# Performance work log

Measured on AMD Instinct MI355X. Metric: run time of the kernel, lower is better.

The kernel has to match this reference:

```python
import jax, jax.numpy as jnp
import numpy as np

TS = 0.1
ECNUM = 1024
CA1NUM = 1024
CA3NUM = 1024
CA3SIGMA = 5.0
TRACKLEN = 100
ACTNUM = 2
BS = 8192
CUELOC = int(0.1 * TRACKLEN)  # sensory cue injected at this step
NOISE_P = 0.04 * TS           # per-step EC3 spontaneous-spike probability


def _xavier_std(fan_in, fan_out):
    return float(np.sqrt(2.0 / (fan_in + fan_out)))


def setup_inputs() -> dict:
    key = jax.random.key(0)
    ks = jax.random.split(key, 6)
    cue = jax.random.normal(ks[0], (BS, ECNUM), jnp.float32)
    ec5_init = jax.random.uniform(ks[1], (BS, ECNUM), jnp.float32)
    wca3ca1 = jax.random.uniform(ks[2], (CA3NUM, CA1NUM), jnp.float32) * 0.01
    wec3ca1 = jax.random.normal(ks[3], (ECNUM, CA1NUM), jnp.float32) * _xavier_std(ECNUM, CA1NUM)
    wca1ec5 = jax.random.normal(ks[4], (CA1NUM, ECNUM), jnp.float32) * _xavier_std(CA1NUM, ECNUM)
    wca1act = jax.random.normal(ks[5], (CA1NUM, ACTNUM), jnp.float32) * _xavier_std(CA1NUM, ACTNUM)
    ca1bias = jnp.zeros((CA1NUM,), jnp.float32)
    ec5bias = jnp.zeros((ECNUM,), jnp.float32)
    actbias = jnp.zeros((ACTNUM,), jnp.float32)
    return {"cue": cue, "ec5_init": ec5_init, "wca3ca1": wca3ca1,
            "wec3ca1": wec3ca1, "wca1ec5": wca1ec5, "wca1act": wca1act,
            "ca1bias": ca1bias, "ec5bias": ec5bias, "actbias": actbias}


def _forward(cue, ec5_init, wca3ca1, wec3ca1, wca1ec5, wca1act, ca1bias, ec5bias, actbias):
    bs = cue.shape[0]
    dt = cue.dtype
    # CA3 place-cell tuning curves for all positions: (T, ca3num)
    ca3center = jnp.linspace(0.0, TRACKLEN, CA3NUM).astype(dt)
    xs = jnp.arange(TRACKLEN)
    ca3_all = jnp.exp(-((ca3center[None, :] - xs[:, None].astype(dt)) ** 2)
                      / (2.0 * CA3SIGMA ** 2))
    drive = ca3_all @ wca3ca1            # (T, ca1num), precomputed CA3->CA1 drive
    cue_mask = (xs == CUELOC).astype(dt)  # (T,)
    noise_key = jax.random.key(42)

    ec3_0 = jnp.zeros((bs, ECNUM), dt)
    ca1_0 = jnp.zeros((bs, CA1NUM), dt)

    def step(carry, inp):
        ec3, ec5, _ = carry
        d, m, t = inp
        ca1 = jax.nn.relu(d[None, :] * (1.0 + jax.nn.sigmoid(ec3 @ wec3ca1)) - ca1bias)
        ec5 = ec5 + (10.0 * TS) * (ca1 @ wca1ec5) + ec5bias
        ec5 = 0.5 + 0.5 * jax.nn.sigmoid(4.0 * (ec5 - 0.5))
        ec3 = ec5 * ec3 + m * cue
        k = jax.random.fold_in(noise_key, t)
        ec3 = ec3 + 0.2 * jax.random.bernoulli(k, NOISE_P, (bs, ECNUM)).astype(dt)
        return (ec3, ec5, ca1), None

    (ec3, ec5, ca1), _ = jax.lax.scan(step, (ec3_0, ec5_init, ca1_0),
                                      (drive, cue_mask, xs))
    return ca1 @ wca1act + actbias       # (bs, actnum)


def reference(cue, ec5_init, wca3ca1, wec3ca1, wca1ec5, wca1act, ca1bias, ec5bias, actbias):
    return _forward(cue, ec5_init, wca3ca1, wec3ca1, wca1ec5, wca1act,
                    ca1bias, ec5bias, actbias)
```

## Files before the change

kernel.cpp:

```cpp
#include <hip/hip_runtime.h>
#include <stdint.h>

#define BS 8192
#define NDIM 1024
#define T_STEPS 100
#define CUE_T 10
#define BK 64
#define NKT (NDIM / BK)

typedef __attribute__((ext_vector_type(8))) short bf16x8;
typedef __attribute__((ext_vector_type(16))) float f32x16;

__device__ inline uint16_t f32_to_bf16(float f) {
    uint32_t u = __float_as_uint(f);
    uint32_t r = u + 0x7fffu + ((u >> 16) & 1u);
    return (uint16_t)(r >> 16);
}
__device__ inline float bf16_to_f32(uint16_t h) {
    return __uint_as_float(((uint32_t)h) << 16);
}

__host__ __device__ inline uint32_t rotl32_(uint32_t x, uint32_t r) {
    return (x << r) | (x >> (32u - r));
}

__host__ __device__ inline void tf2x32(uint32_t k0, uint32_t k1,
                                       uint32_t x0, uint32_t x1,
                                       uint32_t &o0, uint32_t &o1) {
    uint32_t ks2 = k0 ^ k1 ^ 0x1BD11BDAu;
    x0 += k0; x1 += k1;
#define TF_R4(a,b,c,d) \
    x0 += x1; x1 = rotl32_(x1,(a)); x1 ^= x0; \
    x0 += x1; x1 = rotl32_(x1,(b)); x1 ^= x0; \
    x0 += x1; x1 = rotl32_(x1,(c)); x1 ^= x0; \
    x0 += x1; x1 = rotl32_(x1,(d)); x1 ^= x0;
    TF_R4(13,15,26,6)  x0 += k1;  x1 += ks2 + 1u;
    TF_R4(17,29,16,24) x0 += ks2; x1 += k0 + 2u;
    TF_R4(13,15,26,6)  x0 += k0;  x1 += k1 + 3u;
    TF_R4(17,29,16,24) x0 += k1;  x1 += ks2 + 4u;
    TF_R4(13,15,26,6)  x0 += ks2; x1 += k0 + 5u;
#undef TF_R4
    o0 = x0; o1 = x1;
}

__device__ __forceinline__ void tf2x32_x4_fold(uint32_t k0, uint32_t k1,
                                               const uint32_t idx[4],
                                               uint32_t bits[4]) {
    uint32_t ks2 = k0 ^ k1 ^ 0x1BD11BDAu;
    uint32_t x0[4], x1[4];
    #pragma unroll
    for (int i = 0; i < 4; ++i) { x0[i] = k0; x1[i] = idx[i] + k1; }
#define TF4_R(rot) \
    _Pragma("unroll") \
    for (int i = 0; i < 4; ++i) { \
        x0[i] += x1[i]; x1[i] = rotl32_(x1[i], (rot)); x1[i] ^= x0[i]; }
#define TF4_K(a0, a1) \
    _Pragma("unroll") \
    for (int i = 0; i < 4; ++i) { x0[i] += (a0); x1[i] += (a1); }
    TF4_R(13) TF4_R(15) TF4_R(26) TF4_R(6)  TF4_K(k1, ks2 + 1u)
    TF4_R(17) TF4_R(29) TF4_R(16) TF4_R(24) TF4_K(ks2, k0 + 2u)
    TF4_R(13) TF4_R(15) TF4_R(26) TF4_R(6)  TF4_K(k0, k1 + 3u)
    TF4_R(17) TF4_R(29) TF4_R(16) TF4_R(24) TF4_K(k1, ks2 + 4u)
    TF4_R(13) TF4_R(15) TF4_R(26) TF4_R(6)  TF4_K(ks2, k0 + 5u)
#undef TF4_R
#undef TF4_K
    #pragma unroll
    for (int i = 0; i < 4; ++i) bits[i] = x0[i] ^ x1[i];
}

__device__ inline float sigmoidf_(float x) {
    float e = __expf(-x);
    return __builtin_amdgcn_rcpf(1.0f + e);
}

__device__ __forceinline__ void gload16(const uint16_t* g, uint16_t* l) {
    __builtin_amdgcn_global_load_lds(
        (const __attribute__((address_space(1))) void*)g,
        (__attribute__((address_space(3))) void*)l, 16, 0, 0);
}

__global__ void init_kernel(const float* __restrict__ ec5_init,
                            uint16_t* __restrict__ ec3bf,
                            uint16_t* __restrict__ ec5bf, int n) {
    int i = blockIdx.x * blockDim.x + threadIdx.x;
    if (i < n) { ec3bf[i] = 0; ec5bf[i] = f32_to_bf16(ec5_init[i]); }
}

__global__ __launch_bounds__(256) void drive_kernel(const float* __restrict__ W,
                                                    float* __restrict__ drive) {
    __shared__ float g[4][1024];
    const int t0 = blockIdx.x * 4;
    const int c = blockIdx.y * 64 + (threadIdx.x & 63);
    const int tt = threadIdx.x >> 6;
    const float stepf = 100.0f / 1023.0f;
    for (int i = threadIdx.x; i < 4096; i += 256) {
        int t_ = i >> 10, j = i & 1023;
        float d = stepf * (float)j - (float)(t0 + t_);
        g[t_][j] = expf(-(d * d) * 0.02f);
    }
    __syncthreads();
    float a = 0.f;
    for (int j = 0; j < 1024; ++j)
        a = fmaf(g[tt][j], W[(size_t)j * NDIM + c], a);
    drive[(size_t)(t0 + tt) * NDIM + c] = a;
}

__global__ __launch_bounds__(256) void wtrans_kernel(const float* __restrict__ W,
                                                     uint16_t* __restrict__ Wt) {
    __shared__ float tile[32][33];
    int k0 = blockIdx.x * 32, n0 = blockIdx.y * 32;
    int tx = threadIdx.x & 31, ty = threadIdx.x >> 5;
    #pragma unroll
    for (int i = 0; i < 32; i += 8)
        tile[ty + i][tx] = W[(size_t)(k0 + ty + i) * NDIM + n0 + tx];
    __syncthreads();
    #pragma unroll
    for (int i = 0; i < 32; i += 8)
        Wt[(size_t)(n0 + ty + i) * NDIM + k0 + tx] = f32_to_bf16(tile[tx][ty + i]);
}

template<bool NOISE>
__device__ __forceinline__ void gemm_core_t(const uint16_t* __restrict__ A,
                                            const uint16_t* __restrict__ Bt,
                                            uint16_t* As, uint16_t* Bs,
                                            f32x16 acc[2],
                                            uint32_t k0_, uint32_t k1_,
                                            uint32_t obase, uint32_t &mask) {
    const int tid = threadIdx.x;
    const int wid = tid >> 6, lane = tid & 63;
    const int row0 = blockIdx.x * 128, col0 = blockIdx.y * 128;
    const int ch0 = tid, ch1 = tid + 512;
    const int r0c = ch0 >> 3, r1c = ch1 >> 3;
    const int s0 = ((ch0 & 7) ^ (r0c & 7)) << 3;
    const int s1 = ((ch1 & 7) ^ (r1c & 7)) << 3;
    const uint16_t* aS0 = A  + (size_t)(row0 + r0c) * NDIM + s0;
    const uint16_t* aS1 = A  + (size_t)(row0 + r1c) * NDIM + s1;
    const uint16_t* bS0 = Bt + (size_t)(col0 + r0c) * NDIM + s0;
    const uint16_t* bS1 = Bt + (size_t)(col0 + r1c) * NDIM + s1;
    const int l31 = lane & 31, l5 = lane >> 5;
    const int wr = wid >> 1, wc = wid & 1;
    const int ar = wr * 32 + l31;
    int aoff[4], boff[2][4];
    #pragma unroll
    for (int kk = 0; kk < 4; ++kk) {
        aoff[kk] = ar * BK + ((((kk << 1) | l5) ^ (ar & 7)) << 3);
        #pragma unroll
        for (int n = 0; n < 2; ++n) {
            int br = wc * 64 + n * 32 + l31;
            boff[n][kk] = br * BK + ((((kk << 1) | l5) ^ (br & 7)) << 3);
        }
    }

    gload16(aS0, As + ch0 * 8);
    gload16(aS1, As + ch1 * 8);
    gload16(bS0, Bs + ch0 * 8);
    gload16(bS1, Bs + ch1 * 8);

    for (int kt = 0; kt < NKT; ++kt) {
        const int cur = kt & 1;
        if (kt + 1 < NKT) {
            const int nb = (cur ^ 1) * 8192;
            const int k0n = (kt + 1) * BK;
            gload16(aS0 + k0n, As + nb + ch0 * 8);
            gload16(aS1 + k0n, As + nb + ch1 * 8);
            gload16(bS0 + k0n, Bs + nb + ch0 * 8);
            gload16(bS1 + k0n, Bs + nb + ch1 * 8);
            asm volatile("s_waitcnt vmcnt(4)" ::: "memory");
        } else {
            asm volatile("s_waitcnt vmcnt(0)" ::: "memory");
        }
        __builtin_amdgcn_s_barrier();
        __builtin_amdgcn_sched_barrier(0);
        const uint16_t* as = As + cur * 8192;
        const uint16_t* bs = Bs + cur * 8192;
        bf16x8 af[4], bfr[2][4];
        #pragma unroll
        for (int kk = 0; kk < 4; ++kk) {
            af[kk] = *(const bf16x8*)&as[aoff[kk]];
            #pragma unroll
            for (int n = 0; n < 2; ++n)
                bfr[n][kk] = *(const bf16x8*)&bs[boff[n][kk]];
        }
        #pragma unroll
        for (int kk = 0; kk < 4; ++kk)
            #pragma unroll
            for (int n = 0; n < 2; ++n)
                acc[n] = __builtin_amdgcn_mfma_f32_32x32x16_bf16(
                    af[kk], bfr[n][kk], acc[n], 0, 0, 0);
        if (NOISE && !(kt & 1)) {
            uint32_t idx[4], bits[4];
            #pragma unroll
            for (int u = 0; u < 4; ++u) {
                int e = (kt << 1) + u;
                idx[u] = obase + (uint32_t)((e >> 3) << 15) + (uint32_t)(e & 7);
            }
            tf2x32_x4_fold(k0_, k1_, idx, bits);
            #pragma unroll
            for (int u = 0; u < 4; ++u) {
                float uu = __uint_as_float((bits[u] >> 9) | 0x3f800000u) - 1.0f;
                mask |= (uint32_t)(uu < 0.004f ? 1u : 0u) << ((kt << 1) + u);
            }
        }
        __builtin_amdgcn_sched_barrier(0);
        __builtin_amdgcn_s_barrier();
    }
}

__device__ __forceinline__ void acc_to_lds(float* lacc, f32x16 acc[2]) {
    const int tid = threadIdx.x, wid = tid >> 6, lane = tid & 63;
    const int wr = wid >> 1, wc = wid & 1, l31 = lane & 31, l5 = lane >> 5;
    #pragma unroll
    for (int n = 0; n < 2; ++n) {
        int c = wc * 64 + n * 32 + l31;
        int chunk = c >> 2, cj = c & 3;
        #pragma unroll
        for (int e = 0; e < 16; ++e) {
            int r = wr * 32 + (e & 3) + ((e >> 2) << 3) + (l5 << 2);
            lacc[r * 128 + ((chunk ^ (r & 31)) << 2) + cj] = acc[n][e];
        }
    }
}

__device__ __forceinline__ void acc_read8(const float* lacc, int r, int a,
                                          float4 &v0, float4 &v1) {
    int rb = r & 31;
    v0 = *(const float4*)&lacc[r * 128 + ((((a << 1) | 0) ^ rb) << 2)];
    v1 = *(const float4*)&lacc[r * 128 + ((((a << 1) | 1) ^ rb) << 2)];
}

__global__ __launch_bounds__(512, 4) void gemm1_kernel(
    const uint16_t* __restrict__ ec3bf, const uint16_t* __restrict__ W1t,
    const float* __restrict__ drv, const float* __restrict__ bias,
    uint16_t* __restrict__ ca1bf, float* __restrict__ ca1f, int writef32,
    uint32_t* __restrict__ maskbuf, uint32_t k0_, uint32_t k1_)
{
    __shared__ __align__(16) uint16_t SM[2][16384];
    uint16_t* As = SM[0];
    uint16_t* Bs = SM[1];
    f32x16 acc[2];
    acc[0] = (f32x16)(0.0f);
    acc[1] = (f32x16)(0.0f);

    const int tid = threadIdx.x;
    const int row0 = blockIdx.x * 128, col0 = blockIdx.y * 128;
    const int a = tid & 15;
    const uint32_t obase = (uint32_t)(row0 + (tid >> 4)) * NDIM
                         + (uint32_t)(col0 + a * 8);
    uint32_t mask = 0;
    gemm_core_t<true>(ec3bf, W1t, As, Bs, acc, k0_, k1_, obase, mask);

    maskbuf[(size_t)(blockIdx.y * 64 + blockIdx.x) * 512 + tid] = mask;

    float* lacc = (float*)SM;
    acc_to_lds(lacc, acc);
    __syncthreads();

    int gc = col0 + a * 8;
    float4 d0 = *(const float4*)&drv[gc];
    float4 d1 = *(const float4*)&drv[gc + 4];
    float4 b0 = *(const float4*)&bias[gc];
    float4 b1 = *(const float4*)&bias[gc + 4];
    #pragma unroll
    for (int i = 0; i < 4; ++i) {
        int r = (tid >> 4) + i * 32;
        float4 v0, v1;
        acc_read8(lacc, r, a, v0, v1);
        size_t off = (size_t)(row0 + r) * NDIM + gc;
        float vout[8];
        #pragma unroll
        for (int j = 0; j < 8; ++j) {
            float accv = j < 4 ? v0[j] : v1[j - 4];
            float dv = j < 4 ? d0[j] : d1[j - 4];
            float bi = j < 4 ? b0[j] : b1[j - 4];
            float s = sigmoidf_(accv);
            float v = dv * (1.0f + s) - bi;
            vout[j] = v > 0.0f ? v : 0.0f;
        }
        bf16x8 pk;
        #pragma unroll
        for (int j = 0; j < 8; ++j) pk[j] = (short)f32_to_bf16(vout[j]);
        *(bf16x8*)&ca1bf[off] = pk;
        if (writef32) {
            float4 f0 = {vout[0], vout[1], vout[2], vout[3]};
            float4 f1 = {vout[4], vout[5], vout[6], vout[7]};
            *(float4*)&ca1f[off] = f0;
            *(float4*)&ca1f[off + 4] = f1;
        }
    }
}

__global__ __launch_bounds__(512, 4) void gemm2_kernel(
    const uint16_t* __restrict__ ca1bf, const uint16_t* __restrict__ W2t,
    const float* __restrict__ cue, const float* __restrict__ bias,
    uint16_t* __restrict__ ec3bf, uint16_t* __restrict__ ec5bf,
    const uint32_t* __restrict__ maskbuf, int inject)
{
    __shared__ __align__(16) uint16_t SM[2][16384];
    uint16_t* As = SM[0];
    uint16_t* Bs = SM[1];
    f32x16 acc[2];
    acc[0] = (f32x16)(0.0f);
    acc[1] = (f32x16)(0.0f);

    const int tid = threadIdx.x;
    const int row0 = blockIdx.x * 128, col0 = blockIdx.y * 128;
    const int a = tid & 15;
    const uint32_t mask = maskbuf[(size_t)(blockIdx.y * 64 + blockIdx.x) * 512 + tid];

    uint32_t dummy = 0;
    gemm_core_t<false>(ca1bf, W2t, As, Bs, acc, 0u, 0u, 0u, dummy);

    bf16x8 e3v[4], e5v[4];
    #pragma unroll
    for (int i = 0; i < 4; ++i) {
        size_t off = (size_t)(row0 + (tid >> 4) + i * 32) * NDIM + col0 + a * 8;
        e3v[i] = *(const bf16x8*)&ec3bf[off];
        e5v[i] = *(const bf16x8*)&ec5bf[off];
    }

    float* lacc = (float*)SM;
    acc_to_lds(lacc, acc);
    __syncthreads();

    int gc = col0 + a * 8;
    float4 b0 = *(const float4*)&bias[gc];
    float4 b1 = *(const float4*)&bias[gc + 4];
    #pragma unroll
    for (int i = 0; i < 4; ++i) {
        int r = (tid >> 4) + i * 32;
        float4 v0, v1;
        acc_read8(lacc, r, a, v0, v1);
        size_t off = (size_t)(row0 + r) * NDIM + gc;
        float4 c0 = {0.f,0.f,0.f,0.f}, c1 = {0.f,0.f,0.f,0.f};
        if (inject) {
            c0 = *(const float4*)&cue[off];
            c1 = *(const float4*)&cue[off + 4];
        }
        bf16x8 p3, p5;
        #pragma unroll
        for (int j = 0; j < 8; ++j) {
            float accv = j < 4 ? v0[j] : v1[j - 4];
            float bi = j < 4 ? b0[j] : b1[j - 4];
            float e5 = bf16_to_f32((uint16_t)e5v[i][j]);
            float e3 = bf16_to_f32((uint16_t)e3v[i][j]);
            float u = e5 + accv + bi;
            float e5n = 0.5f + 0.5f * sigmoidf_(4.0f * (u - 0.5f));
            float e3n = e5n * e3;
            if (inject) e3n += (j < 4 ? c0[j] : c1[j - 4]);
            e3n += ((mask >> (i * 8 + j)) & 1u) ? 0.2f : 0.0f;
            p5[j] = (short)f32_to_bf16(e5n);
            p3[j] = (short)f32_to_bf16(e3n);
        }
        *(bf16x8*)&ec5bf[off] = p5;
        *(bf16x8*)&ec3bf[off] = p3;
    }
}

__global__ __launch_bounds__(256) void final_kernel(
    const float* __restrict__ ca1,
    const float* __restrict__ wact,
    const float* __restrict__ actbias,
    float* __restrict__ out)
{
    int wave = threadIdx.x >> 6, lane = threadIdx.x & 63;
    int b = blockIdx.x * 4 + wave;
    double a0 = 0.0, a1 = 0.0;
    for (int c = lane; c < NDIM; c += 64) {
        double v = (double)ca1[(size_t)b * NDIM + c];
        a0 += v * (double)wact[c * 2 + 0];
        a1 += v * (double)wact[c * 2 + 1];
    }
    #pragma unroll
    for (int off = 32; off > 0; off >>= 1) {
        a0 += __shfl_down(a0, off);
        a1 += __shfl_down(a1, off);
    }
    if (lane == 0) {
        out[(size_t)b * 2 + 0] = (float)(a0 + (double)actbias[0]);
        out[(size_t)b * 2 + 1] = (float)(a1 + (double)actbias[1]);
    }
}

extern "C" void kernel_launch(void* const* d_in, const int* in_sizes, int n_in,
                              void* d_out, int out_size, void* d_ws, size_t ws_size,
                              hipStream_t stream) {
    const float* cue      = (const float*)d_in[0];
    const float* ec5_init = (const float*)d_in[1];
    const float* wca3ca1  = (const float*)d_in[2];
    const float* wec3ca1  = (const float*)d_in[3];
    const float* wca1ec5  = (const float*)d_in[4];
    const float* wca1act  = (const float*)d_in[5];
    const float* ca1bias  = (const float*)d_in[6];
    const float* ec5bias  = (const float*)d_in[7];
    const float* actbias  = (const float*)d_in[8];
    float* out = (float*)d_out;

    const size_t NE = (size_t)BS * NDIM;
    char* p = (char*)d_ws;
    float*    ca1f    = (float*)p;    p += NE * 4;
    uint16_t* ec3bf   = (uint16_t*)p; p += NE * 2;
    uint16_t* ec5bf   = (uint16_t*)p; p += NE * 2;
    uint16_t* ca1bf   = (uint16_t*)p; p += NE * 2;
    uint16_t* W1t     = (uint16_t*)p; p += (size_t)NDIM * NDIM * 2;
    uint16_t* W2t     = (uint16_t*)p; p += (size_t)NDIM * NDIM * 2;
    uint32_t* maskbuf = (uint32_t*)p; p += (size_t)512 * 512 * 4;
    float*    drive   = (float*)p;

    const int n = (int)NE;
    hipLaunchKernelGGL(init_kernel, dim3((n + 255) / 256), dim3(256), 0, stream,
                       ec5_init, ec3bf, ec5bf, n);
    hipLaunchKernelGGL(drive_kernel, dim3(25, 16), dim3(256), 0, stream,
                       wca3ca1, drive);
    hipLaunchKernelGGL(wtrans_kernel, dim3(32, 32), dim3(256), 0, stream, wec3ca1, W1t);
    hipLaunchKernelGGL(wtrans_kernel, dim3(32, 32), dim3(256), 0, stream, wca1ec5, W2t);

    dim3 blk(512);
    dim3 gg(BS / 128, NDIM / 128);
    for (int t = 0; t < T_STEPS; ++t) {
        uint32_t k0, k1;
        tf2x32(0u, 42u, 0u, (uint32_t)t, k0, k1);
        hipLaunchKernelGGL(gemm1_kernel, gg, blk, 0, stream,
                           ec3bf, W1t, drive + (size_t)t * NDIM, ca1bias,
                           ca1bf, ca1f, (t == T_STEPS - 1) ? 1 : 0,
                           maskbuf, k0, k1);
        if (t < T_STEPS - 1) {
            hipLaunchKernelGGL(gemm2_kernel, gg, blk, 0, stream,
                               ca1bf, W2t, cue, ec5bias, ec3bf, ec5bf,
                               maskbuf, (t == CUE_T) ? 1 : 0);
        }
    }
    hipLaunchKernelGGL(final_kernel, dim3(BS / 4), dim3(256), 0, stream,
                       ca1f, wca1act, actbias, out);
}
```

Baseline: 6.559 ms.

## Shrink GEMM tiles to 128x64 with BK=32 and 256-thread blocks

Retiles both step GEMMs from 128x128 tiles with 512 threads and BK=64 to 128x64 tiles with 256 threads and BK=32. Each wave now computes a 64x32 sub-tile, and LDS shrinks to 32KB per block, so more blocks can be resident and the grid holds twice as many blocks. The noise-mask generation, LDS swizzles, epilogue indexing and mask buffer layout are remapped to match. In exchange there is less data reuse per tile, more K iterations with more barriers, and more global traffic for the A operand.

```diff
diff --git a/kernel.cpp b/kernel.cpp
--- a/kernel.cpp
+++ b/kernel.cpp
@@ -5,7 +5,7 @@
 #define NDIM 1024
 #define T_STEPS 100
 #define CUE_T 10
-#define BK 64
+#define BK 32
 #define NKT (NDIM / BK)
 
 typedef __attribute__((ext_vector_type(8))) short bf16x8;
@@ -122,83 +122,81 @@
 template<bool NOISE>
 __device__ __forceinline__ void gemm_core_t(const uint16_t* __restrict__ A,
                                             const uint16_t* __restrict__ Bt,
-                                            uint16_t* As, uint16_t* Bs,
+                                            uint16_t* SM,
                                             f32x16 acc[2],
                                             uint32_t k0_, uint32_t k1_,
                                             uint32_t obase, uint32_t &mask) {
     const int tid = threadIdx.x;
     const int wid = tid >> 6, lane = tid & 63;
-    const int row0 = blockIdx.x * 128, col0 = blockIdx.y * 128;
-    const int ch0 = tid, ch1 = tid + 512;
-    const int r0c = ch0 >> 3, r1c = ch1 >> 3;
-    const int s0 = ((ch0 & 7) ^ (r0c & 7)) << 3;
-    const int s1 = ((ch1 & 7) ^ (r1c & 7)) << 3;
-    const uint16_t* aS0 = A  + (size_t)(row0 + r0c) * NDIM + s0;
-    const uint16_t* aS1 = A  + (size_t)(row0 + r1c) * NDIM + s1;
-    const uint16_t* bS0 = Bt + (size_t)(col0 + r0c) * NDIM + s0;
-    const uint16_t* bS1 = Bt + (size_t)(col0 + r1c) * NDIM + s1;
+    const int row0 = blockIdx.x * 128, col0 = blockIdx.y * 64;
+    uint16_t* As = SM;
+    uint16_t* Bs = SM + 8192;
+
+    const int soff = (((tid & 3) ^ ((tid >> 2) & 3))) << 3;
+    const uint16_t* aS0 = A  + (size_t)(row0 + (tid >> 2)) * NDIM + soff;
+    const uint16_t* aS1 = A  + (size_t)(row0 + (tid >> 2) + 64) * NDIM + soff;
+    const uint16_t* bS0 = Bt + (size_t)(col0 + (tid >> 2)) * NDIM + soff;
+
     const int l31 = lane & 31, l5 = lane >> 5;
     const int wr = wid >> 1, wc = wid & 1;
-    const int ar = wr * 32 + l31;
-    int aoff[4], boff[2][4];
-    #pragma unroll
-    for (int kk = 0; kk < 4; ++kk) {
-        aoff[kk] = ar * BK + ((((kk << 1) | l5) ^ (ar & 7)) << 3);
-        #pragma unroll
-        for (int n = 0; n < 2; ++n) {
-            int br = wc * 64 + n * 32 + l31;
-            boff[n][kk] = br * BK + ((((kk << 1) | l5) ^ (br & 7)) << 3);
-        }
-    }
-
-    gload16(aS0, As + ch0 * 8);
-    gload16(aS1, As + ch1 * 8);
-    gload16(bS0, Bs + ch0 * 8);
-    gload16(bS1, Bs + ch1 * 8);
+    int aoff[2][2], boff[2];
+    #pragma unroll
+    for (int kk = 0; kk < 2; ++kk) {
+        #pragma unroll
+        for (int m = 0; m < 2; ++m) {
+            int ar = wr * 64 + m * 32 + l31;
+            aoff[m][kk] = ar * BK + ((((kk << 1) | l5) ^ (ar & 3)) << 3);
+        }
+        int br = wc * 32 + l31;
+        boff[kk] = br * BK + ((((kk << 1) | l5) ^ (br & 3)) << 3);
+    }
+
+    gload16(aS0, As + tid * 8);
+    gload16(aS1, As + (tid + 256) * 8);
+    gload16(bS0, Bs + tid * 8);
 
     for (int kt = 0; kt < NKT; ++kt) {
         const int cur = kt & 1;
         if (kt + 1 < NKT) {
-            const int nb = (cur ^ 1) * 8192;
             const int k0n = (kt + 1) * BK;
-            gload16(aS0 + k0n, As + nb + ch0 * 8);
-            gload16(aS1 + k0n, As + nb + ch1 * 8);
-            gload16(bS0 + k0n, Bs + nb + ch0 * 8);
-            gload16(bS1 + k0n, Bs + nb + ch1 * 8);
-            asm volatile("s_waitcnt vmcnt(4)" ::: "memory");
+            uint16_t* An = As + (cur ^ 1) * 4096;
+            uint16_t* Bn = Bs + (cur ^ 1) * 2048;
+            gload16(aS0 + k0n, An + tid * 8);
+            gload16(aS1 + k0n, An + (tid + 256) * 8);
+            gload16(bS0 + k0n, Bn + tid * 8);
+            asm volatile("s_waitcnt vmcnt(3)" ::: "memory");
         } else {
             asm volatile("s_waitcnt vmcnt(0)" ::: "memory");
         }
         __builtin_amdgcn_s_barrier();
         __builtin_amdgcn_sched_barrier(0);
-        const uint16_t* as = As + cur * 8192;
-        const uint16_t* bs = Bs + cur * 8192;
-        bf16x8 af[4], bfr[2][4];
-        #pragma unroll
-        for (int kk = 0; kk < 4; ++kk) {
-            af[kk] = *(const bf16x8*)&as[aoff[kk]];
+        const uint16_t* as = As + cur * 4096;
+        const uint16_t* bs = Bs + cur * 2048;
+        bf16x8 af[2][2], bfr[2];
+        #pragma unroll
+        for (int kk = 0; kk < 2; ++kk) {
+            af[0][kk] = *(const bf16x8*)&as[aoff[0][kk]];
+            af[1][kk] = *(const bf16x8*)&as[aoff[1][kk]];
+            bfr[kk]   = *(const bf16x8*)&bs[boff[kk]];
+        }
+        #pragma unroll
+        for (int kk = 0; kk < 2; ++kk)
             #pragma unroll
-            for (int n = 0; n < 2; ++n)
-                bfr[n][kk] = *(const bf16x8*)&bs[boff[n][kk]];
-        }
-        #pragma unroll
-        for (int kk = 0; kk < 4; ++kk)
+            for (int m = 0; m < 2; ++m)
+                acc[m] = __builtin_amdgcn_mfma_f32_32x32x16_bf16(
+                    af[m][kk], bfr[kk], acc[m], 0, 0, 0);
+        if (NOISE && !(kt & 3)) {
+            const int b = kt >> 2;
+            uint32_t idx[4], bits[4];
+            const uint32_t base = obase + (uint32_t)((b >> 1) << 15)
+                                + (uint32_t)((b & 1) << 2);
             #pragma unroll
-            for (int n = 0; n < 2; ++n)
-                acc[n] = __builtin_amdgcn_mfma_f32_32x32x16_bf16(
-                    af[kk], bfr[n][kk], acc[n], 0, 0, 0);
-        if (NOISE && !(kt & 1)) {
-            uint32_t idx[4], bits[4];
-            #pragma unroll
-            for (int u = 0; u < 4; ++u) {
-                int e = (kt << 1) + u;
-                idx[u] = obase + (uint32_t)((e >> 3) << 15) + (uint32_t)(e & 7);
-            }
+            for (int u = 0; u < 4; ++u) idx[u] = base + u;
             tf2x32_x4_fold(k0_, k1_, idx, bits);
             #pragma unroll
             for (int u = 0; u < 4; ++u) {
                 float uu = __uint_as_float((bits[u] >> 9) | 0x3f800000u) - 1.0f;
-                mask |= (uint32_t)(uu < 0.004f ? 1u : 0u) << ((kt << 1) + u);
+                mask |= (uint32_t)(uu < 0.004f ? 1u : 0u) << ((b << 2) + u);
             }
         }
         __builtin_amdgcn_sched_barrier(0);
@@ -209,47 +207,44 @@
 __device__ __forceinline__ void acc_to_lds(float* lacc, f32x16 acc[2]) {
     const int tid = threadIdx.x, wid = tid >> 6, lane = tid & 63;
     const int wr = wid >> 1, wc = wid & 1, l31 = lane & 31, l5 = lane >> 5;
-    #pragma unroll
-    for (int n = 0; n < 2; ++n) {
-        int c = wc * 64 + n * 32 + l31;
-        int chunk = c >> 2, cj = c & 3;
+    const int c = wc * 32 + l31;
+    const int chunk = c >> 2, cj = c & 3;
+    #pragma unroll
+    for (int m = 0; m < 2; ++m)
         #pragma unroll
         for (int e = 0; e < 16; ++e) {
-            int r = wr * 32 + (e & 3) + ((e >> 2) << 3) + (l5 << 2);
-            lacc[r * 128 + ((chunk ^ (r & 31)) << 2) + cj] = acc[n][e];
-        }
-    }
+            int r = wr * 64 + m * 32 + (e & 3) + ((e >> 2) << 3) + (l5 << 2);
+            lacc[r * 64 + ((chunk ^ (r & 15)) << 2) + cj] = acc[m][e];
+        }
 }
 
 __device__ __forceinline__ void acc_read8(const float* lacc, int r, int a,
                                           float4 &v0, float4 &v1) {
-    int rb = r & 31;
-    v0 = *(const float4*)&lacc[r * 128 + ((((a << 1) | 0) ^ rb) << 2)];
-    v1 = *(const float4*)&lacc[r * 128 + ((((a << 1) | 1) ^ rb) << 2)];
-}
-
-__global__ __launch_bounds__(512, 4) void gemm1_kernel(
+    int rb = r & 15;
+    v0 = *(const float4*)&lacc[r * 64 + ((((a << 1) | 0) ^ rb) << 2)];
+    v1 = *(const float4*)&lacc[r * 64 + ((((a << 1) | 1) ^ rb) << 2)];
+}
+
+__global__ __launch_bounds__(256, 4) void gemm1_kernel(
     const uint16_t* __restrict__ ec3bf, const uint16_t* __restrict__ W1t,
     const float* __restrict__ drv, const float* __restrict__ bias,
     uint16_t* __restrict__ ca1bf, float* __restrict__ ca1f, int writef32,
     uint32_t* __restrict__ maskbuf, uint32_t k0_, uint32_t k1_)
 {
-    __shared__ __align__(16) uint16_t SM[2][16384];
-    uint16_t* As = SM[0];
-    uint16_t* Bs = SM[1];
+    __shared__ __align__(16) uint16_t SM[16384];
     f32x16 acc[2];
     acc[0] = (f32x16)(0.0f);
     acc[1] = (f32x16)(0.0f);
 
     const int tid = threadIdx.x;
-    const int row0 = blockIdx.x * 128, col0 = blockIdx.y * 128;
-    const int a = tid & 15;
-    const uint32_t obase = (uint32_t)(row0 + (tid >> 4)) * NDIM
+    const int row0 = blockIdx.x * 128, col0 = blockIdx.y * 64;
+    const int a = tid & 7;
+    const uint32_t obase = (uint32_t)(row0 + (tid >> 3)) * NDIM
                          + (uint32_t)(col0 + a * 8);
     uint32_t mask = 0;
-    gemm_core_t<true>(ec3bf, W1t, As, Bs, acc, k0_, k1_, obase, mask);
-
-    maskbuf[(size_t)(blockIdx.y * 64 + blockIdx.x) * 512 + tid] = mask;
+    gemm_core_t<true>(ec3bf, W1t, SM, acc, k0_, k1_, obase, mask);
+
+    maskbuf[(size_t)(blockIdx.y * 64 + blockIdx.x) * 256 + tid] = mask;
 
     float* lacc = (float*)SM;
     acc_to_lds(lacc, acc);
@@ -262,7 +257,7 @@
     float4 b1 = *(const float4*)&bias[gc + 4];
     #pragma unroll
     for (int i = 0; i < 4; ++i) {
-        int r = (tid >> 4) + i * 32;
+        int r = (tid >> 3) + i * 32;
         float4 v0, v1;
         acc_read8(lacc, r, a, v0, v1);
         size_t off = (size_t)(row0 + r) * NDIM + gc;
@@ -289,31 +284,29 @@
     }
 }
 
-__global__ __launch_bounds__(512, 4) void gemm2_kernel(
+__global__ __launch_bounds__(256, 4) void gemm2_kernel(
     const uint16_t* __restrict__ ca1bf, const uint16_t* __restrict__ W2t,
     const float* __restrict__ cue, const float* __restrict__ bias,
     uint16_t* __restrict__ ec3bf, uint16_t* __restrict__ ec5bf,
     const uint32_t* __restrict__ maskbuf, int inject)
 {
-    __shared__ __align__(16) uint16_t SM[2][16384];
-    uint16_t* As = SM[0];
-    uint16_t* Bs = SM[1];
+    __shared__ __align__(16) uint16_t SM[16384];
     f32x16 acc[2];
     acc[0] = (f32x16)(0.0f);
     acc[1] = (f32x16)(0.0f);
 
     const int tid = threadIdx.x;
-    const int row0 = blockIdx.x * 128, col0 = blockIdx.y * 128;
-    const int a = tid & 15;
-    const uint32_t mask = maskbuf[(size_t)(blockIdx.y * 64 + blockIdx.x) * 512 + tid];
+    const int row0 = blockIdx.x * 128, col0 = blockIdx.y * 64;
+    const int a = tid & 7;
+    const uint32_t mask = maskbuf[(size_t)(blockIdx.y * 64 + blockIdx.x) * 256 + tid];
 
     uint32_t dummy = 0;
-    gemm_core_t<false>(ca1bf, W2t, As, Bs, acc, 0u, 0u, 0u, dummy);
+    gemm_core_t<false>(ca1bf, W2t, SM, acc, 0u, 0u, 0u, dummy);
 
     bf16x8 e3v[4], e5v[4];
     #pragma unroll
     for (int i = 0; i < 4; ++i) {
-        size_t off = (size_t)(row0 + (tid >> 4) + i * 32) * NDIM + col0 + a * 8;
+        size_t off = (size_t)(row0 + (tid >> 3) + i * 32) * NDIM + col0 + a * 8;
         e3v[i] = *(const bf16x8*)&ec3bf[off];
         e5v[i] = *(const bf16x8*)&ec5bf[off];
     }
@@ -327,7 +320,7 @@
     float4 b1 = *(const float4*)&bias[gc + 4];
     #pragma unroll
     for (int i = 0; i < 4; ++i) {
-        int r = (tid >> 4) + i * 32;
+        int r = (tid >> 3) + i * 32;
         float4 v0, v1;
         acc_read8(lacc, r, a, v0, v1);
         size_t off = (size_t)(row0 + r) * NDIM + gc;
@@ -403,7 +396,7 @@
     uint16_t* ca1bf   = (uint16_t*)p; p += NE * 2;
     uint16_t* W1t     = (uint16_t*)p; p += (size_t)NDIM * NDIM * 2;
     uint16_t* W2t     = (uint16_t*)p; p += (size_t)NDIM * NDIM * 2;
-    uint32_t* maskbuf = (uint32_t*)p; p += (size_t)512 * 512 * 4;
+    uint32_t* maskbuf = (uint32_t*)p; p += (size_t)1024 * 256 * 4;
     float*    drive   = (float*)p;
 
     const int n = (int)NE;
@@ -414,8 +407,8 @@
     hipLaunchKernelGGL(wtrans_kernel, dim3(32, 32), dim3(256), 0, stream, wec3ca1, W1t);
     hipLaunchKernelGGL(wtrans_kernel, dim3(32, 32), dim3(256), 0, stream, wca1ec5, W2t);
 
-    dim3 blk(512);
-    dim3 gg(BS / 128, NDIM / 128);
+    dim3 blk(256);
+    dim3 gg(BS / 128, NDIM / 64);
     for (int t = 0; t < T_STEPS; ++t) {
         uint32_t k0, k1;
         tf2x32(0u, 42u, 0u, (uint32_t)t, k0, k1);
@@ -429,6 +422,6 @@
                                maskbuf, (t == CUE_T) ? 1 : 0);
         }
     }
-    hipLaunchKernelGGL(final_kernel, dim3(BS / 4), dim3(256), 0, stream,
+    hipLaunchKernelGGL(final_kernel, dim3(BS / 4), blk, 0, stream,
                        ca1f, wca1act, actbias, out);
 }
```

Result: slower. 7.809 ms (+19.1%).
